# Kernel optimization log

Measured on AMD Instinct MI355X. Metric: run time of the kernel, lower is better.

The kernel has to match this reference:

```python
import jax, jax.numpy as jnp
import numpy as np
from jax import lax

FRAMES, BATCH, IN_DIM = 512, 2048, 84
HIDDEN, OUT_DIM = 300, 10


def setup_inputs() -> dict:
    key = jax.random.key(0)
    k1, k2, k3, k4 = jax.random.split(key, 4)
    hand_data = jax.random.normal(k1, (FRAMES, BATCH, IN_DIM), dtype=jnp.float32)
    hidden_state = jnp.zeros((BATCH, HIDDEN), dtype=jnp.float32)
    # Linear weights (PyTorch convention: y = x @ W.T), Kaiming-uniform-ish scale
    Wi = jax.random.normal(k2, (HIDDEN, IN_DIM), dtype=jnp.float32) / np.sqrt(IN_DIM)
    Wh = jax.random.normal(k3, (HIDDEN, HIDDEN), dtype=jnp.float32) / np.sqrt(HIDDEN)
    Wo = jax.random.normal(k4, (OUT_DIM, HIDDEN), dtype=jnp.float32) / np.sqrt(HIDDEN)
    return {"hand_data": hand_data, "hidden_state": hidden_state,
            "Wi": Wi, "Wh": Wh, "Wo": Wo}


def reference(hand_data, hidden_state, Wi, Wh, Wo):
    # Precompute the input projection for all frames in one big GEMM:
    # [F,B,I] x [H,I] -> [F,B,H]
    x_proj = jnp.einsum('fbi,hi->fbh', hand_data, Wi)

    def step(h, xp):
        # Elman cell: h' = tanh(i2h(x) + h2h(h))
        h = jnp.tanh(xp + h @ Wh.T)
        return h, None

    h_final, _ = lax.scan(step, hidden_state, x_proj)
    # h2o is computed every iteration in the original, but only the last
    # value is returned, so computing it once on the final hidden state
    # yields identical output.
    out = h_final @ Wo.T  # [B, OUT_DIM]
    return out, h_final
```

## Files before the change

### kernel.cpp

```cpp
#include <hip/hip_runtime.h>
#include <hip/hip_bf16.h>

#define FRAMES 512
#define BATCH 2048
#define IN_DIM 84
#define HIDDEN 300
#define OUT_DIM 10

#define MT 16
#define RSTR 512
#define XK 300
#define KF 12
#define BUFS (MT * RSTR)
#define NT 3

typedef __attribute__((ext_vector_type(8))) short s8v;
typedef __attribute__((ext_vector_type(4))) short s4v;
typedef __attribute__((ext_vector_type(4))) float f4v;

__device__ __forceinline__ short f2b(float x) {
    __hip_bfloat16 h = __float2bfloat16(x);
    return *reinterpret_cast<short*>(&h);
}
__device__ __forceinline__ float b2f(short s) {
    __hip_bfloat16 h = *reinterpret_cast<__hip_bfloat16*>(&s);
    return __bfloat162float(h);
}
__device__ __forceinline__ float fast_tanh(float z) {
    float ex = __builtin_amdgcn_exp2f(z * 2.88539008177792681f);
    return fmaf(-2.f, __builtin_amdgcn_rcpf(ex + 1.f), 1.f);
}
__device__ __forceinline__ int g(int r, int c) {
    return r * RSTR + ((r & 7) << 3) + c;
}
__device__ __forceinline__ void lgkm_barrier() {
    asm volatile("s_waitcnt lgkmcnt(0)" ::: "memory");
    __builtin_amdgcn_s_barrier();
}


__global__ __launch_bounds__(512, 2)
void rnn_kernel(const float* __restrict__ x, const float* __restrict__ h0,
                const float* __restrict__ Wi, const float* __restrict__ Wh,
                const float* __restrict__ Wo, float* __restrict__ out)
{
    __shared__ short lds[2 * BUFS];
    const int tid  = threadIdx.x;
    const int lane = tid & 63;
    const int wv   = tid >> 6;
    const int l15  = lane & 15;
    const int lkhi = lane >> 4;
    const int b0   = blockIdx.x * MT;
    const bool w3  = (wv < 3);
    const bool t18mask = (wv != 2) || (lkhi != 3);

    s8v w[NT][KF];
#pragma unroll
    for (int i = 0; i < NT; ++i) {
        const int n = (wv + 8 * i) * 16 + l15;
#pragma unroll
        for (int kf = 0; kf < KF; ++kf) {
            s8v v;
#pragma unroll
            for (int j = 0; j < 8; ++j) {
                int k = kf * 32 + lkhi * 8 + j;
                float f = 0.f;
                if (n < HIDDEN) f = (k < XK) ? Wh[n * HIDDEN + k] : Wi[n * IN_DIM + (k - XK)];
                v[j] = f2b(f);
            }
            w[i][kf] = v;
        }
    }

    {
        s4v z = (s4v){0, 0, 0, 0};
        for (int i = tid; i < 2 * BUFS / 4; i += 512)
            ((s4v*)lds)[i] = z;
    }
    __syncthreads();

    for (int i = tid; i < MT * HIDDEN; i += 512) {
        int r = i / HIDDEN, c = i % HIDDEN;
        lds[g(r, c)] = f2b(h0[(size_t)(b0 + r) * HIDDEN + c]);
    }
    if (tid < 336) {
        const float4* xs = reinterpret_cast<const float4*>(x + (size_t)b0 * IN_DIM);
        float4 v0 = xs[tid];
        int r = tid / 21, c4 = (tid % 21) * 4;
        s4v pk = {f2b(v0.x), f2b(v0.y), f2b(v0.z), f2b(v0.w)};
        *reinterpret_cast<s4v*>(&lds[g(r, XK + c4)]) = pk;
    }

    const int rdh   = g(l15, lkhi * 8);
    const int wrb   = g(l15, lkhi * 4);
    const int xti   = (tid < 336) ? tid : 0;
    const int xcb1  = g(xti / 21, XK + (xti % 21) * 4);
    const bool xact = (tid < 336);
    const f4v zero4 = (f4v){0.f, 0.f, 0.f, 0.f};

    float4 xa0, xb0;
    xa0 = reinterpret_cast<const float4*>(x + ((size_t)BATCH + b0) * IN_DIM)[xti];
    __syncthreads();

#define STEP(PH, SF, A0, B0, LOADF, COMMITF)                                    \
    {                                                                           \
        if (LOADF) {                                                            \
            B0 = reinterpret_cast<const float4*>(                               \
                x + ((size_t)((SF) + 2) * BATCH + b0) * IN_DIM)[xti];           \
        }                                                                       \
        s8v bf[KF];                                                             \
        _Pragma("unroll")                                                       \
        for (int kf = 0; kf < KF; ++kf)                                         \
            bf[kf] = *(const s8v*)&lds[(PH) * BUFS + rdh + kf * 32];            \
        __builtin_amdgcn_s_setprio(1);                                          \
        if (w3) {                                                               \
            f4v a0 = __builtin_amdgcn_mfma_f32_16x16x32_bf16(w[0][0], bf[0], zero4, 0, 0, 0); \
            f4v a1 = __builtin_amdgcn_mfma_f32_16x16x32_bf16(w[1][0], bf[0], zero4, 0, 0, 0); \
            f4v a2 = __builtin_amdgcn_mfma_f32_16x16x32_bf16(w[2][0], bf[0], zero4, 0, 0, 0); \
            _Pragma("unroll")                                                   \
            for (int kf = 1; kf < KF; ++kf) {                                   \
                a0 = __builtin_amdgcn_mfma_f32_16x16x32_bf16(w[0][kf], bf[kf], a0, 0, 0, 0); \
                a1 = __builtin_amdgcn_mfma_f32_16x16x32_bf16(w[1][kf], bf[kf], a1, 0, 0, 0); \
                a2 = __builtin_amdgcn_mfma_f32_16x16x32_bf16(w[2][kf], bf[kf], a2, 0, 0, 0); \
            }                                                                   \
            __builtin_amdgcn_s_setprio(0);                                      \
            s4v h0v, h1v, h2v;                                                  \
            _Pragma("unroll")                                                   \
            for (int r = 0; r < 4; ++r) {                                       \
                h0v[r] = f2b(fast_tanh(a0[r]));                                 \
                h1v[r] = f2b(fast_tanh(a1[r]));                                 \
                h2v[r] = f2b(fast_tanh(a2[r]));                                 \
            }                                                                   \
            *(s4v*)&lds[((PH) ^ 1) * BUFS + wrb + (wv)      * 16] = h0v;        \
            *(s4v*)&lds[((PH) ^ 1) * BUFS + wrb + (wv + 8)  * 16] = h1v;        \
            if (t18mask)                                                        \
                *(s4v*)&lds[((PH) ^ 1) * BUFS + wrb + (wv + 16) * 16] = h2v;    \
        } else {                                                                \
            f4v a0 = __builtin_amdgcn_mfma_f32_16x16x32_bf16(w[0][0], bf[0], zero4, 0, 0, 0); \
            f4v a1 = __builtin_amdgcn_mfma_f32_16x16x32_bf16(w[1][0], bf[0], zero4, 0, 0, 0); \
            _Pragma("unroll")                                                   \
            for (int kf = 1; kf < KF; ++kf) {                                   \
                a0 = __builtin_amdgcn_mfma_f32_16x16x32_bf16(w[0][kf], bf[kf], a0, 0, 0, 0); \
                a1 = __builtin_amdgcn_mfma_f32_16x16x32_bf16(w[1][kf], bf[kf], a1, 0, 0, 0); \
            }                                                                   \
            __builtin_amdgcn_s_setprio(0);                                      \
            s4v h0v, h1v;                                                       \
            _Pragma("unroll")                                                   \
            for (int r = 0; r < 4; ++r) {                                       \
                h0v[r] = f2b(fast_tanh(a0[r]));                                 \
                h1v[r] = f2b(fast_tanh(a1[r]));                                 \
            }                                                                   \
            *(s4v*)&lds[((PH) ^ 1) * BUFS + wrb + (wv)     * 16] = h0v;         \
            *(s4v*)&lds[((PH) ^ 1) * BUFS + wrb + (wv + 8) * 16] = h1v;         \
        }                                                                       \
        if ((COMMITF) && xact) {                                                \
            s4v pk = {f2b(A0.x), f2b(A0.y), f2b(A0.z), f2b(A0.w)};              \
            *(s4v*)&lds[((PH) ^ 1) * BUFS + xcb1] = pk;                         \
        }                                                                       \
        lgkm_barrier();                                                         \
    }

    for (int s = 0; s < FRAMES - 2; s += 2) {
        STEP(0, s,     xa0, xb0, 1, 1)
        STEP(1, s + 1, xb0, xa0, 1, 1)
    }
    STEP(0, 510, xa0, xb0, 0, 1)
    STEP(1, 511, xb0, xa0, 0, 0)
#undef STEP

    float* hout = out + BATCH * OUT_DIM;
    for (int i = tid; i < MT * HIDDEN; i += 512) {
        int r = i / HIDDEN, c = i % HIDDEN;
        hout[(size_t)(b0 + r) * HIDDEN + c] = b2f(lds[g(r, c)]);
    }
    if (tid < MT * OUT_DIM) {
        int r = tid / OUT_DIM, c = tid % OUT_DIM;
        float sum = 0.f;
        for (int k = 0; k < HIDDEN; ++k)
            sum = fmaf(b2f(lds[g(r, k)]), Wo[c * HIDDEN + k], sum);
        out[(b0 + r) * OUT_DIM + c] = sum;
    }
}

extern "C" void kernel_launch(void* const* d_in, const int* in_sizes, int n_in,
                              void* d_out, int out_size, void* d_ws, size_t ws_size,
                              hipStream_t stream) {
    const float* x  = (const float*)d_in[0];
    const float* h0 = (const float*)d_in[1];
    const float* Wi = (const float*)d_in[2];
    const float* Wh = (const float*)d_in[3];
    const float* Wo = (const float*)d_in[4];
    float* out = (float*)d_out;
    rnn_kernel<<<dim3(BATCH / MT), dim3(512), 0, stream>>>(x, h0, Wi, Wh, Wo, out);
}
```

Baseline: 529.4 us.

## Quantize hidden state and recurrent weights to int8 MFMA, keep input in bf16

The recurrent matmul now runs on int8 MFMA (16x16x64). Wh is quantized per-tensor with a scale found by a max reduction, and the hidden state is stored as int8 in LDS at a fixed 1/127 scale. The input projection stays as a separate bf16 MFMA path with its own LDS region. The aim is to halve the LDS read traffic and the MFMA count per step on the serial critical path. In exchange, the hidden state and Wh lose a lot of precision, which may break output tolerance.

```diff
diff --git a/kernel.cpp b/kernel.cpp
--- a/kernel.cpp
+++ b/kernel.cpp
@@ -8,43 +8,51 @@
 #define OUT_DIM 10
 
 #define MT 16
-#define RSTR 512
-#define XK 300
-#define KF 12
-#define BUFS (MT * RSTR)
+#define HROW 512
+#define XOFF 8192
+#define XROW 512
+#define BUFB 16384
+#define KFH 5
+#define KFX 3
 #define NT 3
 
 typedef __attribute__((ext_vector_type(8))) short s8v;
 typedef __attribute__((ext_vector_type(4))) short s4v;
 typedef __attribute__((ext_vector_type(4))) float f4v;
+typedef __attribute__((ext_vector_type(4))) int   i4v;
 
 __device__ __forceinline__ short f2b(float x) {
     __hip_bfloat16 h = __float2bfloat16(x);
     return *reinterpret_cast<short*>(&h);
 }
-__device__ __forceinline__ float b2f(short s) {
-    __hip_bfloat16 h = *reinterpret_cast<__hip_bfloat16*>(&s);
-    return __bfloat162float(h);
-}
 __device__ __forceinline__ float fast_tanh(float z) {
     float ex = __builtin_amdgcn_exp2f(z * 2.88539008177792681f);
     return fmaf(-2.f, __builtin_amdgcn_rcpf(ex + 1.f), 1.f);
 }
-__device__ __forceinline__ int g(int r, int c) {
-    return r * RSTR + ((r & 7) << 3) + c;
-}
 __device__ __forceinline__ void lgkm_barrier() {
     asm volatile("s_waitcnt lgkmcnt(0)" ::: "memory");
     __builtin_amdgcn_s_barrier();
 }
 
+
+#define MFI(T, K, ACC) ACC = __builtin_amdgcn_mfma_i32_16x16x64_i8(wq[T][K], bh[K], ACC, 0, 0, 0)
+#define MFX(T, K, ACC) ACC = __builtin_amdgcn_mfma_f32_16x16x32_bf16(wx[T][K], bx[K], ACC, 0, 0, 0)
+#define TAIL(AI, AF, IDX, COND) do { unsigned pk_ = 0;                          \
+        _Pragma("unroll")                                                       \
+        for (int r_ = 0; r_ < 4; ++r_) {                                        \
+            float pre_ = fmaf(qs, (float)AI[r_], AF[r_]);                       \
+            float t_ = fast_tanh(pre_);                                         \
+            pk_ |= (__float_as_uint(fmaf(t_, 127.f, 12582912.f)) & 255u) << (8 * r_); \
+        }                                                                       \
+        if (COND) *(unsigned*)&ldsb[IDX] = pk_; } while (0)
 
 __global__ __launch_bounds__(512, 2)
 void rnn_kernel(const float* __restrict__ x, const float* __restrict__ h0,
                 const float* __restrict__ Wi, const float* __restrict__ Wh,
                 const float* __restrict__ Wo, float* __restrict__ out)
 {
-    __shared__ short lds[2 * BUFS];
+    __shared__ __align__(16) char ldsb[2 * BUFB];
+    __shared__ float redbuf[8];
     const int tid  = threadIdx.x;
     const int lane = tid & 63;
     const int wv   = tid >> 6;
@@ -54,49 +62,81 @@
     const bool w3  = (wv < 3);
     const bool t18mask = (wv != 2) || (lkhi != 3);
 
-    s8v w[NT][KF];
+    float m = 0.f;
+    for (int i = tid; i < HIDDEN * HIDDEN; i += 512)
+        m = fmaxf(m, fabsf(Wh[i]));
+#pragma unroll
+    for (int o = 32; o; o >>= 1) m = fmaxf(m, __shfl_xor(m, o));
+    if (lane == 0) redbuf[wv] = m;
+    __syncthreads();
+    float gm = 0.f;
+#pragma unroll
+    for (int i = 0; i < 8; ++i) gm = fmaxf(gm, redbuf[i]);
+    const float inv_sw = 127.f / gm;
+    const float qs     = gm / (127.f * 127.f);
+
+    i4v wq[NT][KFH];
+    s8v wx[NT][KFX];
 #pragma unroll
     for (int i = 0; i < NT; ++i) {
         const int n = (wv + 8 * i) * 16 + l15;
 #pragma unroll
-        for (int kf = 0; kf < KF; ++kf) {
+        for (int kf = 0; kf < KFH; ++kf) {
+            int dw0 = 0, dw1 = 0, dw2 = 0, dw3 = 0;
+#pragma unroll
+            for (int j = 0; j < 16; ++j) {
+                int k = kf * 64 + lkhi * 16 + j;
+                float f = (n < HIDDEN && k < HIDDEN) ? Wh[n * HIDDEN + k] : 0.f;
+                int q = (int)rintf(f * inv_sw) & 255;
+                if ((j >> 2) == 0) dw0 |= q << ((j & 3) * 8);
+                else if ((j >> 2) == 1) dw1 |= q << ((j & 3) * 8);
+                else if ((j >> 2) == 2) dw2 |= q << ((j & 3) * 8);
+                else dw3 |= q << ((j & 3) * 8);
+            }
+            wq[i][kf] = (i4v){dw0, dw1, dw2, dw3};
+        }
+#pragma unroll
+        for (int f = 0; f < KFX; ++f) {
             s8v v;
 #pragma unroll
             for (int j = 0; j < 8; ++j) {
-                int k = kf * 32 + lkhi * 8 + j;
-                float f = 0.f;
-                if (n < HIDDEN) f = (k < XK) ? Wh[n * HIDDEN + k] : Wi[n * IN_DIM + (k - XK)];
-                v[j] = f2b(f);
+                int k = f * 32 + lkhi * 8 + j;
+                v[j] = f2b((n < HIDDEN && k < IN_DIM) ? Wi[n * IN_DIM + k] : 0.f);
             }
-            w[i][kf] = v;
+            wx[i][f] = v;
         }
     }
 
     {
-        s4v z = (s4v){0, 0, 0, 0};
-        for (int i = tid; i < 2 * BUFS / 4; i += 512)
-            ((s4v*)lds)[i] = z;
+        i4v z = (i4v){0, 0, 0, 0};
+        for (int i = tid; i < 2 * BUFB / 16; i += 512)
+            ((i4v*)ldsb)[i] = z;
     }
     __syncthreads();
 
     for (int i = tid; i < MT * HIDDEN; i += 512) {
         int r = i / HIDDEN, c = i % HIDDEN;
-        lds[g(r, c)] = f2b(h0[(size_t)(b0 + r) * HIDDEN + c]);
+        float h = h0[(size_t)(b0 + r) * HIDDEN + c];
+        ldsb[r * HROW + ((r & 7) << 4) + c] =
+            (char)(__float_as_uint(fmaf(h, 127.f, 12582912.f)) & 255u);
     }
     if (tid < 336) {
         const float4* xs = reinterpret_cast<const float4*>(x + (size_t)b0 * IN_DIM);
         float4 v0 = xs[tid];
-        int r = tid / 21, c4 = (tid % 21) * 4;
+        int r = tid / 21, c = tid % 21;
         s4v pk = {f2b(v0.x), f2b(v0.y), f2b(v0.z), f2b(v0.w)};
-        *reinterpret_cast<s4v*>(&lds[g(r, XK + c4)]) = pk;
-    }
-
-    const int rdh   = g(l15, lkhi * 8);
-    const int wrb   = g(l15, lkhi * 4);
-    const int xti   = (tid < 336) ? tid : 0;
-    const int xcb1  = g(xti / 21, XK + (xti % 21) * 4);
+        *reinterpret_cast<s4v*>(&ldsb[XOFF + r * XROW + ((r & 7) << 4) + c * 8]) = pk;
+    }
+
+    const int hrd = l15 * HROW + ((l15 & 7) << 4) + lkhi * 16;
+    const int hwr = l15 * HROW + ((l15 & 7) << 4) + lkhi * 4;
+    const int xrd = XOFF + l15 * XROW + ((l15 & 7) << 4) + lkhi * 16;
+    const int xti = (tid < 336) ? tid : 0;
+    const int xr_ = xti / 21, xc_ = xti % 21;
+    const int xcb = XOFF + xr_ * XROW + ((xr_ & 7) << 4) + xc_ * 8;
     const bool xact = (tid < 336);
     const f4v zero4 = (f4v){0.f, 0.f, 0.f, 0.f};
+    const i4v zeroi = (i4v){0, 0, 0, 0};
 
     float4 xa0, xb0;
     xa0 = reinterpret_cast<const float4*>(x + ((size_t)BATCH + b0) * IN_DIM)[xti];
@@ -108,54 +148,53 @@
             B0 = reinterpret_cast<const float4*>(                               \
                 x + ((size_t)((SF) + 2) * BATCH + b0) * IN_DIM)[xti];           \
         }                                                                       \
-        s8v bf[KF];                                                             \
+        if ((COMMITF) && xact) {                                                \
+            s4v pk = {f2b(A0.x), f2b(A0.y), f2b(A0.z), f2b(A0.w)};              \
+            *(s4v*)&ldsb[((PH) ^ 1) * BUFB + xcb] = pk;                         \
+        }                                                                       \
+        i4v bh[KFH]; s8v bx[KFX];                                               \
         _Pragma("unroll")                                                       \
-        for (int kf = 0; kf < KF; ++kf)                                         \
-            bf[kf] = *(const s8v*)&lds[(PH) * BUFS + rdh + kf * 32];            \
+        for (int kf = 0; kf < KFH; ++kf)                                        \
+            bh[kf] = *(const i4v*)&ldsb[(PH) * BUFB + hrd + kf * 64];           \
+        _Pragma("unroll")                                                       \
+        for (int f = 0; f < KFX; ++f)                                           \
+            bx[f] = *(const s8v*)&ldsb[(PH) * BUFB + xrd + f * 64];             \
         __builtin_amdgcn_s_setprio(1);                                          \
         if (w3) {                                                               \
-            f4v a0 = __builtin_amdgcn_mfma_f32_16x16x32_bf16(w[0][0], bf[0], zero4, 0, 0, 0); \
-            f4v a1 = __builtin_amdgcn_mfma_f32_16x16x32_bf16(w[1][0], bf[0], zero4, 0, 0, 0); \
-            f4v a2 = __builtin_amdgcn_mfma_f32_16x16x32_bf16(w[2][0], bf[0], zero4, 0, 0, 0); \
-            _Pragma("unroll")                                                   \
-            for (int kf = 1; kf < KF; ++kf) {                                   \
-                a0 = __builtin_amdgcn_mfma_f32_16x16x32_bf16(w[0][kf], bf[kf], a0, 0, 0, 0); \
-                a1 = __builtin_amdgcn_mfma_f32_16x16x32_bf16(w[1][kf], bf[kf], a1, 0, 0, 0); \
-                a2 = __builtin_amdgcn_mfma_f32_16x16x32_bf16(w[2][kf], bf[kf], a2, 0, 0, 0); \
+            i4v a0i = __builtin_amdgcn_mfma_i32_16x16x64_i8(wq[0][0], bh[0], zeroi, 0, 0, 0); \
+            i4v a1i = __builtin_amdgcn_mfma_i32_16x16x64_i8(wq[1][0], bh[0], zeroi, 0, 0, 0); \
+            i4v a2i = __builtin_amdgcn_mfma_i32_16x16x64_i8(wq[2][0], bh[0], zeroi, 0, 0, 0); \
+            _Pragma("unroll")                                                   \
+            for (int kf = 1; kf < KFH; ++kf) {                                  \
+                MFI(0, kf, a0i); MFI(1, kf, a1i); MFI(2, kf, a2i);              \
+            }                                                                   \
+            f4v a0f = __builtin_amdgcn_mfma_f32_16x16x32_bf16(wx[0][0], bx[0], zero4, 0, 0, 0); \
+            f4v a1f = __builtin_amdgcn_mfma_f32_16x16x32_bf16(wx[1][0], bx[0], zero4, 0, 0, 0); \
+            f4v a2f = __builtin_amdgcn_mfma_f32_16x16x32_bf16(wx[2][0], bx[0], zero4, 0, 0, 0); \
+            _Pragma("unroll")                                                   \
+            for (int f = 1; f < KFX; ++f) {                                     \
+                MFX(0, f, a0f); MFX(1, f, a1f); MFX(2, f, a2f);                 \
             }                                                                   \
             __builtin_amdgcn_s_setprio(0);                                      \
-            s4v h0v, h1v, h2v;                                                  \
-            _Pragma("unroll")                                                   \
-            for (int r = 0; r < 4; ++r) {                                       \
-                h0v[r] = f2b(fast_tanh(a0[r]));                                 \
-                h1v[r] = f2b(fast_tanh(a1[r]));                                 \
-                h2v[r] = f2b(fast_tanh(a2[r]));                                 \
-            }                                                                   \
-            *(s4v*)&lds[((PH) ^ 1) * BUFS + wrb + (wv)      * 16] = h0v;        \
-            *(s4v*)&lds[((PH) ^ 1) * BUFS + wrb + (wv + 8)  * 16] = h1v;        \
-            if (t18mask)                                                        \
-                *(s4v*)&lds[((PH) ^ 1) * BUFS + wrb + (wv + 16) * 16] = h2v;    \
+            TAIL(a0i, a0f, ((PH) ^ 1) * BUFB + hwr + (wv) * 16, true);          \
+            TAIL(a1i, a1f, ((PH) ^ 1) * BUFB + hwr + (wv + 8) * 16, true);      \
+            TAIL(a2i, a2f, ((PH) ^ 1) * BUFB + hwr + (wv + 16) * 16, t18mask);  \
         } else {                                                                \
-            f4v a0 = __builtin_amdgcn_mfma_f32_16x16x32_bf16(w[0][0], bf[0], zero4, 0, 0, 0); \
-            f4v a1 = __builtin_amdgcn_mfma_f32_16x16x32_bf16(w[1][0], bf[0], zero4, 0, 0, 0); \
-            _Pragma("unroll")                                                   \
-            for (int kf = 1; kf < KF; ++kf) {                                   \
-                a0 = __builtin_amdgcn_mfma_f32_16x16x32_bf16(w[0][kf], bf[kf], a0, 0, 0, 0); \
-                a1 = __builtin_amdgcn_mfma_f32_16x16x32_bf16(w[1][kf], bf[kf], a1, 0, 0, 0); \
+            i4v a0i = __builtin_amdgcn_mfma_i32_16x16x64_i8(wq[0][0], bh[0], zeroi, 0, 0, 0); \
+            i4v a1i = __builtin_amdgcn_mfma_i32_16x16x64_i8(wq[1][0], bh[0], zeroi, 0, 0, 0); \
+            _Pragma("unroll")                                                   \
+            for (int kf = 1; kf < KFH; ++kf) {                                  \
+                MFI(0, kf, a0i); MFI(1, kf, a1i);                               \
+            }                                                                   \
+            f4v a0f = __builtin_amdgcn_mfma_f32_16x16x32_bf16(wx[0][0], bx[0], zero4, 0, 0, 0); \
+            f4v a1f = __builtin_amdgcn_mfma_f32_16x16x32_bf16(wx[1][0], bx[0], zero4, 0, 0, 0); \
+            _Pragma("unroll")                                                   \
+            for (int f = 1; f < KFX; ++f) {                                     \
+                MFX(0, f, a0f); MFX(1, f, a1f);                                 \
             }                                                                   \
             __builtin_amdgcn_s_setprio(0);                                      \
-            s4v h0v, h1v;                                                       \
-            _Pragma("unroll")                                                   \
-            for (int r = 0; r < 4; ++r) {                                       \
-                h0v[r] = f2b(fast_tanh(a0[r]));                                 \
-                h1v[r] = f2b(fast_tanh(a1[r]));                                 \
-            }                                                                   \
-            *(s4v*)&lds[((PH) ^ 1) * BUFS + wrb + (wv)     * 16] = h0v;         \
-            *(s4v*)&lds[((PH) ^ 1) * BUFS + wrb + (wv + 8) * 16] = h1v;         \
-        }                                                                       \
-        if ((COMMITF) && xact) {                                                \
-            s4v pk = {f2b(A0.x), f2b(A0.y), f2b(A0.z), f2b(A0.w)};              \
-            *(s4v*)&lds[((PH) ^ 1) * BUFS + xcb1] = pk;                         \
+            TAIL(a0i, a0f, ((PH) ^ 1) * BUFB + hwr + (wv) * 16, true);          \
+            TAIL(a1i, a1f, ((PH) ^ 1) * BUFB + hwr + (wv + 8) * 16, true);      \
         }                                                                       \
         lgkm_barrier();                                                         \
     }
@@ -168,16 +207,20 @@
     STEP(1, 511, xb0, xa0, 0, 0)
 #undef STEP
 
+    const float dq = 1.f / 127.f;
     float* hout = out + BATCH * OUT_DIM;
     for (int i = tid; i < MT * HIDDEN; i += 512) {
         int r = i / HIDDEN, c = i % HIDDEN;
-        hout[(size_t)(b0 + r) * HIDDEN + c] = b2f(lds[g(r, c)]);
+        hout[(size_t)(b0 + r) * HIDDEN + c] =
+            (float)((int)(signed char)ldsb[r * HROW + ((r & 7) << 4) + c]) * dq;
     }
     if (tid < MT * OUT_DIM) {
         int r = tid / OUT_DIM, c = tid % OUT_DIM;
         float sum = 0.f;
-        for (int k = 0; k < HIDDEN; ++k)
-            sum = fmaf(b2f(lds[g(r, k)]), Wo[c * HIDDEN + k], sum);
+        for (int k = 0; k < HIDDEN; ++k) {
+            float h = (float)((int)(signed char)ldsb[r * HROW + ((r & 7) << 4) + k]) * dq;
+            sum = fmaf(h, Wo[c * HIDDEN + k], sum);
+        }
         out[(b0 + r) * OUT_DIM + c] = sum;
     }
 }
```

Result: no change. 520.5 us (-1.7%).
